# Optimization experiments

Hardware: AMD Instinct MI355X
Metric: run time of the kernel (lower is better)

Reference implementation:

```python
import jax, jax.numpy as jnp
import numpy as np

NC = 19
CH16, CH32 = 1024, 2048
B, H, W = 4, 64, 64
EPS = 1e-5


def bn_relu(x, gamma, beta):
    # Train-mode BatchNorm (batch statistics, as in torch default) + ReLU.
    axes = (0,) + tuple(range(2, x.ndim))  # reduce over batch + spatial
    mean = jnp.mean(x, axes, keepdims=True)
    var = jnp.var(x, axes, keepdims=True)
    shp = (1, -1) + (1,) * (x.ndim - 2)
    return jax.nn.relu((x - mean) * jax.lax.rsqrt(var + EPS) * gamma.reshape(shp) + beta.reshape(shp))


def setup_inputs() -> dict:
    key = jax.random.key(0)
    ks = jax.random.split(key, 10)
    def p(k, shape, fan):
        return jax.random.normal(k, shape, jnp.float32) / np.float32(np.sqrt(fan))
    ones = lambda c: jnp.ones((c,), jnp.float32)
    zeros = lambda c: jnp.zeros((c,), jnp.float32)
    return {
        "x": jax.random.normal(ks[0], (B, CH32, H, W), jnp.float32),
        "low_level_feature": jax.random.normal(ks[1], (B, CH16, H, W), jnp.float32),
        "W_L": p(ks[2], (NC, CH16), CH16), "b_L": zeros(NC),
        "W_X": p(ks[3], (512, CH32, 3, 3), CH32 * 9), "g_X": ones(512), "be_X": zeros(512),
        "W_phi": p(ks[4], (256, 512), 512), "g_phi": ones(256), "be_phi": zeros(256),
        "W_psi": p(ks[5], (256, 512), 512), "g_psi": ones(256), "be_psi": zeros(256),
        "W_delta": p(ks[6], (256, 512), 512), "g_delta": ones(256), "be_delta": zeros(256),
        "W_rho": p(ks[7], (512, 256), 256), "g_rho": ones(512), "be_rho": zeros(512),
        "W_g": p(ks[8], (512, 1024), 1024), "g_g": ones(512), "be_g": zeros(512),
        "W_out": p(ks[9], (NC, 512), 512), "b_out": zeros(NC),
    }


def reference(x, low_level_feature, W_L, b_L, W_X, g_X, be_X,
              W_phi, g_phi, be_phi, W_psi, g_psi, be_psi,
              W_delta, g_delta, be_delta, W_rho, g_rho, be_rho,
              W_g, g_g, be_g, W_out, b_out):
    b, _, h, w = x.shape
    # X = conv2d(2048->512, 3x3) + BN + ReLU
    Xf = jax.lax.conv_general_dilated(x, W_X, (1, 1), 'SAME',
                                      dimension_numbers=('NCHW', 'OIHW', 'NCHW'))
    Xf = bn_relu(Xf, g_X, be_X)                          # [b,512,h,w]
    # L = 1x1 conv (with bias) -> soft object regions
    L = jnp.einsum('bchw,nc->bnhw', low_level_feature, W_L) + b_L[None, :, None, None]
    l_flat = L.reshape(b, L.shape[1], -1)                # [b,nc,N]
    M = jax.nn.softmax(l_flat, axis=-1)                  # softmax over N
    X_flat = Xf.reshape(b, 512, -1)                      # [b,512,N]
    # f_k = (M @ X_flat^T)^T : object region features [b,512,nc]
    f_k = jnp.einsum('bkn,bcn->bck', M, X_flat)
    # phi/psi/delta: 1x1 conv1d + BN + ReLU
    query = bn_relu(jnp.einsum('oc,bck->bok', W_phi, f_k), g_phi, be_phi)      # [b,256,nc]
    key_ = bn_relu(jnp.einsum('oc,bcn->bon', W_psi, X_flat), g_psi, be_psi)    # [b,256,N]
    logit = jnp.einsum('bqk,bqn->bkn', query, key_)      # [b,nc,N]
    attn = jax.nn.softmax(logit, axis=1)                 # softmax over nc (dim 1)
    delta = bn_relu(jnp.einsum('oc,bck->bok', W_delta, f_k), g_delta, be_delta)  # [b,256,nc]
    attn_sum = jnp.einsum('bqk,bkn->bqn', delta, attn)   # [b,256,N]
    X_obj = bn_relu(jnp.einsum('oq,bqn->bon', W_rho, attn_sum), g_rho, be_rho)
    X_obj = X_obj.reshape(b, 512, h, w)
    concat = jnp.concatenate([Xf, X_obj], axis=1)        # [b,1024,h,w]
    X_bar = bn_relu(jnp.einsum('oc,bchw->bohw', W_g, concat), g_g, be_g)
    out = jnp.einsum('nc,bchw->bnhw', W_out, X_bar) + b_out[None, :, None, None]
    return out
```

## Files before the change

kernel.cpp:

```cpp
#include <hip/hip_runtime.h>
#include <hip/hip_bf16.h>
#include <cstdint>
#include <cstddef>

#define EPSV 1e-5f

typedef float f32x4 __attribute__((ext_vector_type(4)));
typedef _Float16 f16x8 __attribute__((ext_vector_type(8)));
typedef unsigned short ushortx8 __attribute__((ext_vector_type(8)));

__device__ __forceinline__ unsigned short f2h(float f) {
  _Float16 h = (_Float16)f;
  return *reinterpret_cast<unsigned short*>(&h);
}

__device__ __forceinline__ void gload16(const void* g, void* l) {
  __builtin_amdgcn_global_load_lds(
      (const __attribute__((address_space(1))) void*)g,
      (__attribute__((address_space(3))) void*)l, 16, 0, 0);
}

__global__ __launch_bounds__(256) void ocr_halo_zero(unsigned short* __restrict__ xT) {
  int e = blockIdx.x, b = blockIdx.y, t = threadIdx.x;
  ushortx8 z = {0, 0, 0, 0, 0, 0, 0, 0};
  if (e < 2) {
    int row = e ? 65 : 0;
    ushortx8* p = (ushortx8*)(xT + (size_t)(b * 66 + row) * 66 * 2048);
    for (int i = t; i < 66 * 256; i += 256) p[i] = z;
  } else {
    int col = (e == 3) ? 65 : 0;
    for (int idx = t; idx < 64 * 256; idx += 256) {
      int r = (idx >> 8) + 1, v = idx & 255;
      ((ushortx8*)(xT + ((size_t)(b * 66 + r) * 66 + col) * 2048))[v] = z;
    }
  }
}

__global__ __launch_bounds__(256) void ocr_cvt_x(const float* __restrict__ x,
                                                 unsigned short* __restrict__ xT) {
  __shared__ float tile[64][65];
  int icb = blockIdx.x, h = blockIdx.y, b = blockIdx.z, t = threadIdx.x;
  const float* xp = x + ((size_t)b * 2048 + icb * 64) * 4096 + h * 64;
  #pragma unroll
  for (int r = 0; r < 16; ++r) {
    int icl = r * 4 + (t >> 6), w = t & 63;
    tile[icl][w] = xp[(size_t)icl * 4096 + w];
  }
  __syncthreads();
  #pragma unroll
  for (int it = 0; it < 2; ++it) {
    int w = it * 32 + (t >> 3), cb = (t & 7) * 8;
    ushortx8 o;
    #pragma unroll
    for (int j = 0; j < 8; ++j) o[j] = f2h(tile[cb + j][w]);
    *(ushortx8*)&xT[(((size_t)b * 66 + h + 1) * 66 + (w + 1)) * 2048 + icb * 64 + cb] = o;
  }
}

__global__ __launch_bounds__(256) void ocr_cvt_w(const float* __restrict__ Wx,
                                                 unsigned short* __restrict__ WT) {
  int oc = blockIdx.x >> 3;
  int ic = (blockIdx.x & 7) * 256 + threadIdx.x;
  const float* wp = Wx + ((size_t)oc * 2048 + ic) * 9;
  float v[9];
  #pragma unroll
  for (int t = 0; t < 9; ++t) v[t] = wp[t];
  #pragma unroll
  for (int t = 0; t < 9; ++t)
    WT[((size_t)t * 512 + oc) * 2048 + ic] = f2h(v[t]);
}

__global__ __launch_bounds__(256) void ocr_cvt_h2(const float* __restrict__ inA,
                                                  unsigned short* __restrict__ outA,
                                                  const float* __restrict__ inB,
                                                  unsigned short* __restrict__ outB) {
  int i = blockIdx.x * 256 + threadIdx.x;
  if (i < 131072) outA[i] = f2h(inA[i]);
  if (i < 524288) outB[i] = f2h(inB[i]);
}

__global__ __launch_bounds__(512, 4) void ocr_conv_mfma(const unsigned short* __restrict__ xT,
                                                        const unsigned short* __restrict__ WT,
                                                        float* __restrict__ Xf) {
  __shared__ __align__(16) char lds_raw[65536];
  float* red = (float*)lds_raw;

  const int t = threadIdx.x;
  const int wv = t >> 6, lane = t & 63;
  const int kg = lane >> 4, lc = lane & 15;
  const int ws = wv & 3, kh = wv >> 2;

  const int bx = blockIdx.x;
  const int hg  = ((bx & 7) << 1) | ((bx >> 3) & 1);
  const int b   = (bx >> 4) & 3;
  const int oct = bx >> 6;
  const int oc0 = oct * 64, h0 = hg * 4;

  const char* gp[8]; int lo[8]; bool go[8];
  #pragma unroll
  for (int i = 0; i < 8; ++i) {
    int c = wv * 8 + i;
    go[i] = c < 63;
    int cc = go[i] ? c : 0;
    if (cc < 38) {
      int cell = cc * 64 + lane; if (cell > 2375) cell = 2375;
      int r = cell / 66, col = cell - r * 66; if (col > 63) col = 63;
      int tap = r >> 2, kgs = r & 3;
      gp[i] = (const char*)WT + (size_t)(((tap * 512 + oc0 + col) * 2048) + kgs * 8) * 2;
      lo[i] = cc * 1024;
    } else {
      int c2 = cc - 38;
      int cell = c2 * 64 + lane; if (cell > 1583) cell = 1583;
      int r = cell / 66, col = cell - r * 66;
      int row = r >> 2, kgs = r & 3;
      gp[i] = (const char*)xT + (size_t)((((b * 66 + h0 + row) * 66 + col) * 2048) + kgs * 8) * 2;
      lo[i] = 38912 + c2 * 1024;
    }
  }

  f32x4 acc[4][4] = {};

  #pragma unroll
  for (int i = 0; i < 8; ++i) if (go[i]) gload16(gp[i], lds_raw + lo[i]);
  __syncthreads();

  #pragma unroll 1
  for (int step = 0; step < 64; ++step) {
    const short* As = (const short*)lds_raw;
    const short* Bs = (const short*)(lds_raw + 38912);
    #pragma unroll
    for (int j = 0; j < 5; ++j) {
      const int tap = kh * 4 + j;
      const int dh = tap / 3, dw = tap - dh * 3;
      f16x8 av[4];
      #pragma unroll
      for (int mi = 0; mi < 4; ++mi)
        av[mi] = *(const f16x8*)&As[((tap * 4 + kg) * 66 + mi * 16 + lc) * 8];
      const int row = ws + dh;
      const int nw0 = (tap == 4) ? (kh ? 2 : 0) : 0;
      const int nwN = (tap == 4) ? (nw0 + 2) : 4;
      #pragma unroll
      for (int nw = 0; nw < 4; ++nw) {
        if (nw >= nw0 && nw < nwN) {
          f16x8 bv = *(const f16x8*)&Bs[((row * 4 + kg) * 66 + nw * 16 + lc + dw) * 8];
          #pragma unroll
          for (int mi = 0; mi < 4; ++mi)
            acc[mi][nw] = __builtin_amdgcn_mfma_f32_16x16x32_f16(av[mi], bv, acc[mi][nw], 0, 0, 0);
        }
      }
    }
    if (step < 63) {
      __syncthreads();
      unsigned adv = (unsigned)(step + 1) * 64u;
      #pragma unroll
      for (int i = 0; i < 8; ++i) if (go[i]) gload16(gp[i] + adv, lds_raw + lo[i]);
      __syncthreads();
    }
  }

  __syncthreads();
  if (kh == 1) {
    #pragma unroll
    for (int mi = 0; mi < 4; ++mi)
      #pragma unroll
      for (int nw = 0; nw < 4; ++nw)
        *(f32x4*)&red[(((ws * 16 + mi * 4 + nw) * 64) + lane) * 4] = acc[mi][nw];
  }
  __syncthreads();
  if (kh == 0) {
    const int h = h0 + ws;
    #pragma unroll
    for (int mi = 0; mi < 4; ++mi) {
      #pragma unroll
      for (int nw = 0; nw < 4; ++nw) {
        f32x4 other = *(const f32x4*)&red[(((ws * 16 + mi * 4 + nw) * 64) + lane) * 4];
        f32x4 s = acc[mi][nw] + other;
        #pragma unroll
        for (int r = 0; r < 4; ++r) {
          int oc = oc0 + mi * 16 + (lane >> 4) * 4 + r;
          int w = nw * 16 + lc;
          Xf[(((size_t)b * 512 + oc) * 64 + h) * 64 + w] = s[r];
        }
      }
    }
  }
}

template<int K, int OT, int NT, int NWM, int NWN, int LDB>
__global__ __launch_bounds__(256) void ocr_gemm_h(const unsigned short* __restrict__ Ah,
                                                  const unsigned short* __restrict__ Bh,
                                                  float* __restrict__ Cm, int O) {
  static_assert(NT == 128, "NT fixed");
  constexpr int MI = OT / NWM / 16;
  constexpr int NI = NT / NWN / 16;
  constexpr int SA = OT + 2, SB = NT + 2;
  constexpr int ACELL = 4 * OT / 256;
  constexpr int ABUF = 4 * SA * 8;
  constexpr int BBUF = 4 * SB * 8;
  constexpr int NS = K / 32;
  constexpr int LPW = ACELL + 2;
  __shared__ __align__(16) short As_s[2 * ABUF];
  __shared__ __align__(16) short Bs_s[2 * BBUF];

  const int t = threadIdx.x;
  const int wv = t >> 6, lane = t & 63;
  const int kg = lane >> 4, lc = lane & 15;
  const int wm = wv / NWN, wn = wv % NWN;

  const int n0 = blockIdx.x * NT, o0 = blockIdx.y * OT, b = blockIdx.z;

  const char* aBase[ACELL]; int aLds[ACELL];
  #pragma unroll
  for (int r = 0; r < ACELL; ++r) {
    int flat0 = r * 256 + (t & 448);
    int flat  = flat0 + lane;
    int kgs = flat / OT, ol = flat % OT;
    aBase[r] = (const char*)(Ah + ((size_t)(o0 + ol)) * K + kgs * 8);
    aLds[r] = ((flat0 / OT) * SA + (flat0 % OT)) * 16;
  }
  const char* bBase[2]; int bLds[2];
  #pragma unroll
  for (int r = 0; r < 2; ++r) {
    int flat0 = r * 256 + (t & 448);
    int flat  = flat0 + lane;
    int kgs = flat >> 7, nl = flat & 127;
    bBase[r] = (const char*)(Bh + ((size_t)b * 4096 + n0 + nl) * LDB + kgs * 8);
    bLds[r] = ((flat0 >> 7) * SB + (flat0 & 127)) * 16;
  }

  f32x4 acc[MI][NI] = {};
  #pragma unroll
  for (int r = 0; r < ACELL; ++r) gload16(aBase[r], (char*)As_s + aLds[r]);
  #pragma unroll
  for (int r = 0; r < 2; ++r) gload16(bBase[r], (char*)Bs_s + bLds[r]);
  asm volatile("s_waitcnt vmcnt(0)" ::: "memory");
  __builtin_amdgcn_s_barrier();

  int cur = 0;
  #pragma unroll 1
  for (int step = 0; step < NS; ++step) {
    if (step + 1 < NS) {
      unsigned adv = (unsigned)(step + 1) * 64u;
      int nA = (cur ^ 1) * ABUF * 2, nB = (cur ^ 1) * BBUF * 2;
      #pragma unroll
      for (int r = 0; r < ACELL; ++r) gload16(aBase[r] + adv, (char*)As_s + nA + aLds[r]);
      #pragma unroll
      for (int r = 0; r < 2; ++r) gload16(bBase[r] + adv, (char*)Bs_s + nB + bLds[r]);
      if constexpr (LPW == 3) asm volatile("s_waitcnt vmcnt(3)" ::: "memory");
      else                    asm volatile("s_waitcnt vmcnt(4)" ::: "memory");
    } else {
      asm volatile("s_waitcnt vmcnt(0)" ::: "memory");
    }
    __builtin_amdgcn_s_barrier();

    const short* As = As_s + cur * ABUF;
    const short* Bsc = Bs_s + cur * BBUF;
    f16x8 av[MI], bv[NI];
    #pragma unroll
    for (int mi = 0; mi < MI; ++mi)
      av[mi] = *(const f16x8*)&As[(kg * SA + wm * (MI * 16) + mi * 16 + lc) * 8];
    #pragma unroll
    for (int ni = 0; ni < NI; ++ni)
      bv[ni] = *(const f16x8*)&Bsc[(kg * SB + wn * (NI * 16) + ni * 16 + lc) * 8];
    __builtin_amdgcn_s_setprio(1);
    #pragma unroll
    for (int mi = 0; mi < MI; ++mi)
      #pragma unroll
      for (int ni = 0; ni < NI; ++ni)
        acc[mi][ni] = __builtin_amdgcn_mfma_f32_16x16x32_f16(av[mi], bv[ni], acc[mi][ni], 0, 0, 0);
    __builtin_amdgcn_s_setprio(0);
    asm volatile("s_waitcnt lgkmcnt(0)" ::: "memory");
    __builtin_amdgcn_sched_barrier(0);
    __builtin_amdgcn_s_barrier();
    cur ^= 1;
  }
  #pragma unroll
  for (int mi = 0; mi < MI; ++mi) {
    #pragma unroll
    for (int ni = 0; ni < NI; ++ni) {
      int n = n0 + wn * (NI * 16) + ni * 16 + lc;
      #pragma unroll
      for (int r = 0; r < 4; ++r) {
        int oc = o0 + wm * (MI * 16) + mi * 16 + (lane >> 4) * 4 + r;
        Cm[((size_t)b * O + oc) * 4096 + n] = acc[mi][ni][r];
      }
    }
  }
}

__global__ __launch_bounds__(256) void ocr_t2h(const float* __restrict__ in,
                                               const float* __restrict__ scale,
                                               const float* __restrict__ shift,
                                               unsigned short* __restrict__ out,
                                               int C, int coff) {
  __shared__ float tile[64][65];
  int n0 = blockIdx.x * 64, c0 = blockIdx.y * 64, b = blockIdx.z;
  int t = threadIdx.x;
  #pragma unroll
  for (int r = 0; r < 16; ++r) {
    int c_l = r * 4 + (t >> 6), n_l = t & 63;
    tile[c_l][n_l] = in[((size_t)(b * C + c0 + c_l)) * 4096 + n0 + n_l];
  }
  __syncthreads();
  int n_l = t >> 2, cb = (t & 3) * 16;
  ushortx8 o0v, o1v;
  #pragma unroll
  for (int j = 0; j < 8; ++j) {
    int c = c0 + cb + j;
    o0v[j] = f2h(fmaxf(0.f, tile[cb + j][n_l] * scale[c] + shift[c]));
  }
  #pragma unroll
  for (int j = 0; j < 8; ++j) {
    int c = c0 + cb + 8 + j;
    o1v[j] = f2h(fmaxf(0.f, tile[cb + 8 + j][n_l] * scale[c] + shift[c]));
  }
  size_t base = ((size_t)b * 4096 + n0 + n_l) * 1024 + coff + c0 + cb;
  *(ushortx8*)&out[base] = o0v;
  *(ushortx8*)&out[base + 8] = o1v;
}

__global__ __launch_bounds__(256) void ocr_chan_stats(const float* __restrict__ buf,
                                                      const float* __restrict__ gamma,
                                                      const float* __restrict__ beta,
                                                      float* __restrict__ scale,
                                                      float* __restrict__ shift, int C) {
  int c = blockIdx.x, t = threadIdx.x;
  float s = 0.f, q = 0.f;
  for (int b = 0; b < 4; ++b) {
    const float* p = buf + ((size_t)b * C + c) * 4096;
    for (int i = t; i < 4096; i += 256) { float v = p[i]; s += v; q += v * v; }
  }
  __shared__ float ls[256], lq[256];
  ls[t] = s; lq[t] = q; __syncthreads();
  for (int off = 128; off > 0; off >>= 1) {
    if (t < off) { ls[t] += ls[t + off]; lq[t] += lq[t + off]; }
    __syncthreads();
  }
  if (t == 0) {
    float mean = ls[0] / 16384.f;
    float var  = lq[0] / 16384.f - mean * mean;
    float sc   = gamma[c] * rsqrtf(var + EPSV);
    scale[c] = sc; shift[c] = beta[c] - mean * sc;
  }
}

__global__ __launch_bounds__(256) void ocr_lproj(const float* __restrict__ llf,
                                                 const float* __restrict__ WL,
                                                 const float* __restrict__ bL,
                                                 float* __restrict__ L) {
  int h = blockIdx.x, b = blockIdx.y;
  int t = threadIdx.x, w = t & 63, csub = t >> 6;
  float acc[19];
  #pragma unroll
  for (int k = 0; k < 19; ++k) acc[k] = 0.f;
  const float* base = llf + ((size_t)b * 1024 + csub * 256) * 4096 + h * 64 + w;
  #pragma unroll 1
  for (int c4 = 0; c4 < 64; ++c4) {
    float lv[4];
    #pragma unroll
    for (int i = 0; i < 4; ++i) lv[i] = base[(size_t)(c4 + i * 64) * 4096];
    #pragma unroll
    for (int i = 0; i < 4; ++i) {
      const float* wl = &WL[csub * 256 + c4 + i * 64];
      #pragma unroll
      for (int k = 0; k < 19; ++k) acc[k] += wl[k * 1024] * lv[i];
    }
  }
  __shared__ float red[4][64][19];
  #pragma unroll
  for (int k = 0; k < 19; ++k) red[csub][w][k] = acc[k];
  __syncthreads();
  if (csub == 0) {
    #pragma unroll
    for (int k = 0; k < 19; ++k) {
      float s = red[0][w][k] + red[1][w][k] + red[2][w][k] + red[3][w][k] + bL[k];
      L[((size_t)b * 19 + k) * 4096 + h * 64 + w] = s;
    }
  }
}

__global__ __launch_bounds__(256) void ocr_softmax4096(float* __restrict__ buf) {
  int row = blockIdx.x, t = threadIdx.x;
  float* p = buf + (size_t)row * 4096;
  __shared__ float ls[256];
  float m = -1e30f;
  for (int i = t; i < 4096; i += 256) m = fmaxf(m, p[i]);
  ls[t] = m; __syncthreads();
  for (int off = 128; off > 0; off >>= 1) { if (t < off) ls[t] = fmaxf(ls[t], ls[t + off]); __syncthreads(); }
  m = ls[0]; __syncthreads();
  float s = 0.f;
  for (int i = t; i < 4096; i += 256) { float e = __expf(p[i] - m); p[i] = e; s += e; }
  ls[t] = s; __syncthreads();
  for (int off = 128; off > 0; off >>= 1) { if (t < off) ls[t] += ls[t + off]; __syncthreads(); }
  float inv = 1.f / ls[0];
  for (int i = t; i < 4096; i += 256) p[i] *= inv;
}

__global__ __launch_bounds__(256) void ocr_fk(const float* __restrict__ M,
                                              const float* __restrict__ Xf,
                                              const float* __restrict__ scale,
                                              const float* __restrict__ shift,
                                              float* __restrict__ fk) {
  int c = blockIdx.x, b = blockIdx.y, t = threadIdx.x;
  float acc[19];
  #pragma unroll
  for (int k = 0; k < 19; ++k) acc[k] = 0.f;
  const float* xp = Xf + ((size_t)b * 512 + c) * 4096;
  const float* mp = M + (size_t)b * 19 * 4096;
  float sc = scale[c], sh = shift[c];
  for (int n = t; n < 4096; n += 256) {
    float xv = fmaxf(0.f, xp[n] * sc + sh);
    #pragma unroll
    for (int k = 0; k < 19; ++k) acc[k] += mp[k * 4096 + n] * xv;
  }
  __shared__ float red[19 * 256];
  #pragma unroll
  for (int k = 0; k < 19; ++k) red[k * 256 + t] = acc[k];
  __syncthreads();
  for (int off = 128; off > 0; off >>= 1) {
    if (t < off) {
      #pragma unroll
      for (int k = 0; k < 19; ++k) red[k * 256 + t] += red[k * 256 + t + off];
    }
    __syncthreads();
  }
  if (t < 19) fk[((size_t)b * 512 + c) * 19 + t] = red[t * 256];
}

__global__ __launch_bounds__(256) void ocr_qd2(const float* __restrict__ Wphi,
                                               const float* __restrict__ Wdelta,
                                               const float* __restrict__ fk,
                                               float* __restrict__ qry,
                                               float* __restrict__ dlt) {
  int blk = blockIdx.x;
  const float* Wm = (blk < 76) ? Wphi : Wdelta;
  float* out = (blk < 76) ? qry : dlt;
  int tid = (blk < 76 ? blk : blk - 76) * 256 + threadIdx.x;
  if (tid >= 4 * 256 * 19) return;
  int k = tid % 19, o = (tid / 19) % 256, b = tid / (19 * 256);
  const float* fp = fk + (size_t)b * 512 * 19 + k;
  const float* wp = Wm + (size_t)o * 512;
  float acc = 0.f;
  for (int c = 0; c < 512; ++c) acc += wp[c] * fp[c * 19];
  out[tid] = acc;
}

__global__ __launch_bounds__(128) void ocr_bn76x2(float* __restrict__ qry,
                                                  float* __restrict__ dlt,
                                                  const float* __restrict__ g_phi,
                                                  const float* __restrict__ be_phi,
                                                  const float* __restrict__ g_delta,
                                                  const float* __restrict__ be_delta) {
  bool second = blockIdx.x >= 256;
  int o = blockIdx.x & 255, t = threadIdx.x;
  float* buf = second ? dlt : qry;
  const float* gamma = second ? g_delta : g_phi;
  const float* beta  = second ? be_delta : be_phi;
  bool act = t < 76;
  float v = 0.f;
  size_t idx = 0;
  if (act) {
    int b = t / 19, k = t % 19;
    idx = ((size_t)b * 256 + o) * 19 + k;
    v = buf[idx];
  }
  __shared__ float ls[128], lq[128];
  ls[t] = act ? v : 0.f; lq[t] = act ? v * v : 0.f; __syncthreads();
  for (int off = 64; off > 0; off >>= 1) { if (t < off) { ls[t] += ls[t + off]; lq[t] += lq[t + off]; } __syncthreads(); }
  __shared__ float s_sc, s_sh;
  if (t == 0) {
    float mean = ls[0] / 76.f;
    float var  = lq[0] / 76.f - mean * mean;
    float sc   = gamma[o] * rsqrtf(var + EPSV);
    s_sc = sc; s_sh = beta[o] - mean * sc;
  }
  __syncthreads();
  if (act) buf[idx] = fmaxf(0.f, v * s_sc + s_sh);
}

__global__ __launch_bounds__(256) void ocr_attn(const float* __restrict__ query,
                                                const float* __restrict__ key,
                                                const float* __restrict__ scale,
                                                const float* __restrict__ shift,
                                                float* __restrict__ attn) {
  int n0 = blockIdx.x * 64, b = blockIdx.y;
  int t = threadIdx.x, nl = t & 63, qsub = t >> 6;
  __shared__ float ql[256 * 19];
  for (int i = t; i < 256 * 19; i += 256) ql[i] = query[(size_t)b * 256 * 19 + i];
  __syncthreads();
  float acc[19];
  #pragma unroll
  for (int k = 0; k < 19; ++k) acc[k] = 0.f;
  const float* kp = key + ((size_t)b * 256 + qsub * 64) * 4096 + n0 + nl;
  #pragma unroll 1
  for (int q4 = 0; q4 < 64; q4 += 4) {
    float kv[4];
    #pragma unroll
    for (int i = 0; i < 4; ++i) kv[i] = kp[(size_t)(q4 + i) * 4096];
    #pragma unroll
    for (int i = 0; i < 4; ++i) {
      int ch = qsub * 64 + q4 + i;
      float kva = fmaxf(0.f, kv[i] * scale[ch] + shift[ch]);
      const float* qq = &ql[ch * 19];
      #pragma unroll
      for (int k = 0; k < 19; ++k) acc[k] += qq[k] * kva;
    }
  }
  __shared__ float red[4][64][19];
  #pragma unroll
  for (int k = 0; k < 19; ++k) red[qsub][nl][k] = acc[k];
  __syncthreads();
  if (qsub == 0) {
    float v[19]; float m = -1e30f;
    #pragma unroll
    for (int k = 0; k < 19; ++k) {
      v[k] = red[0][nl][k] + red[1][nl][k] + red[2][nl][k] + red[3][nl][k];
      m = fmaxf(m, v[k]);
    }
    float s = 0.f;
    #pragma unroll
    for (int k = 0; k < 19; ++k) { v[k] = __expf(v[k] - m); s += v[k]; }
    float inv = 1.f / s;
    #pragma unroll
    for (int k = 0; k < 19; ++k)
      attn[((size_t)b * 19 + k) * 4096 + n0 + nl] = v[k] * inv;
  }
}

__global__ __launch_bounds__(256) void ocr_wd(const float* __restrict__ Wrho,
                                              const float* __restrict__ dlt,
                                              float* __restrict__ Wd) {
  int tid = blockIdx.x * 256 + threadIdx.x;
  if (tid >= 4 * 512 * 19) return;
  int k = tid % 19, o = (tid / 19) % 512, b = tid / (19 * 512);
  const float* dp = dlt + (size_t)b * 256 * 19 + k;
  const float* wp = Wrho + (size_t)o * 256;
  float acc = 0.f;
  for (int q = 0; q < 256; ++q) acc += wp[q] * dp[q * 19];
  Wd[tid] = acc;
}

__global__ __launch_bounds__(384) void ocr_gram(const float* __restrict__ attn,
                                                float* __restrict__ G,
                                                float* __restrict__ RS) {
  __shared__ float al[19][513];
  int n0 = blockIdx.x * 512, b = blockIdx.y, t = threadIdx.x;
  for (int i = t; i < 19 * 512; i += 384) {
    int k = i >> 9, n = i & 511;
    al[k][n] = attn[((size_t)b * 19 + k) * 4096 + n0 + n];
  }
  __syncthreads();
  if (t < 361) {
    int k1 = t / 19, k2 = t % 19;
    float s = 0.f;
    for (int n = 0; n < 512; ++n) s += al[k1][n] * al[k2][n];
    atomicAdd(&G[(b * 19 + k1) * 19 + k2], s);
  } else if (t < 380) {
    int k = t - 361;
    float s = 0.f;
    for (int n = 0; n < 512; ++n) s += al[k][n];
    atomicAdd(&RS[b * 19 + k], s);
  }
}

__global__ __launch_bounds__(512) void ocr_xobj_fin(const float* __restrict__ Wd,
                                                    const float* __restrict__ G,
                                                    const float* __restrict__ RS,
                                                    const float* __restrict__ gamma,
                                                    const float* __restrict__ beta,
                                                    float* __restrict__ scale,
                                                    float* __restrict__ shift) {
  int o = threadIdx.x;
  float s = 0.f, q = 0.f;
  for (int b = 0; b < 4; ++b) {
    float wd[19];
    #pragma unroll
    for (int k = 0; k < 19; ++k) wd[k] = Wd[((size_t)b * 512 + o) * 19 + k];
    const float* g = &G[b * 361];
    const float* rs = &RS[b * 19];
    #pragma unroll
    for (int k = 0; k < 19; ++k) s += wd[k] * rs[k];
    for (int k1 = 0; k1 < 19; ++k1) {
      float tacc = 0.f;
      #pragma unroll
      for (int k2 = 0; k2 < 19; ++k2) tacc += g[k1 * 19 + k2] * wd[k2];
      q += wd[k1] * tacc;
    }
  }
  float mean = s / 16384.f;
  float var  = q / 16384.f - mean * mean;
  float sc   = gamma[o] * rsqrtf(var + EPSV);
  scale[o] = sc; shift[o] = beta[o] - mean * sc;
}

__global__ __launch_bounds__(512) void ocr_xobj_apply(const float* __restrict__ Wd,
                                                      const float* __restrict__ attn,
                                                      const float* __restrict__ scale,
                                                      const float* __restrict__ shift,
                                                      unsigned short* __restrict__ ch) {
  __shared__ float al[19][256];
  int n0 = blockIdx.x * 256, b = blockIdx.y, o = threadIdx.x;
  for (int idx = o; idx < 19 * 256; idx += 512) {
    int k = idx >> 8, nl = idx & 255;
    al[k][nl] = attn[((size_t)b * 19 + k) * 4096 + n0 + nl];
  }
  float wd[19];
  #pragma unroll
  for (int k = 0; k < 19; ++k) wd[k] = Wd[((size_t)b * 512 + o) * 19 + k];
  float sc = scale[o], sh = shift[o];
  __syncthreads();
  #pragma unroll 1
  for (int nl = 0; nl < 256; ++nl) {
    float v = 0.f;
    #pragma unroll
    for (int k = 0; k < 19; ++k) v += wd[k] * al[k][nl];
    v = fmaxf(0.f, v * sc + sh);
    ch[((size_t)b * 4096 + n0 + nl) * 1024 + 512 + o] = f2h(v);
  }
}

__global__ __launch_bounds__(256) void ocr_out(const float* __restrict__ Wout,
                                               const float* __restrict__ bout,
                                               const float* __restrict__ Xbar,
                                               const float* __restrict__ scale,
                                               const float* __restrict__ shift,
                                               float* __restrict__ out) {
  int n0 = blockIdx.x * 64, b = blockIdx.y;
  int t = threadIdx.x, nl = t & 63, csub = t >> 6;
  float acc[19];
  #pragma unroll
  for (int k = 0; k < 19; ++k) acc[k] = 0.f;
  const float* base = Xbar + ((size_t)b * 512 + csub * 128) * 4096 + n0 + nl;
  #pragma unroll 1
  for (int c4 = 0; c4 < 128; c4 += 4) {
    float xv[4];
    #pragma unroll
    for (int i = 0; i < 4; ++i) xv[i] = base[(size_t)(c4 + i) * 4096];
    #pragma unroll
    for (int i = 0; i < 4; ++i) {
      int chn = csub * 128 + c4 + i;
      float a = fmaxf(0.f, xv[i] * scale[chn] + shift[chn]);
      #pragma unroll
      for (int k = 0; k < 19; ++k) acc[k] += Wout[k * 512 + chn] * a;
    }
  }
  __shared__ float red[4][64][19];
  #pragma unroll
  for (int k = 0; k < 19; ++k) red[csub][nl][k] = acc[k];
  __syncthreads();
  if (csub == 0) {
    #pragma unroll
    for (int k = 0; k < 19; ++k) {
      float s = red[0][nl][k] + red[1][nl][k] + red[2][nl][k] + red[3][nl][k] + bout[k];
      out[((size_t)b * 19 + k) * 4096 + n0 + nl] = s;
    }
  }
}

extern "C" void kernel_launch(void* const* d_in, const int* in_sizes, int n_in,
                              void* d_out, int out_size, void* d_ws, size_t ws_size,
                              hipStream_t stream) {
  const float* x    = (const float*)d_in[0];
  const float* llf  = (const float*)d_in[1];
  const float* W_L  = (const float*)d_in[2];
  const float* b_L  = (const float*)d_in[3];
  const float* W_X  = (const float*)d_in[4];
  const float* g_X  = (const float*)d_in[5];
  const float* be_X = (const float*)d_in[6];
  const float* W_phi = (const float*)d_in[7];
  const float* g_phi = (const float*)d_in[8];
  const float* be_phi = (const float*)d_in[9];
  const float* W_psi = (const float*)d_in[10];
  const float* g_psi = (const float*)d_in[11];
  const float* be_psi = (const float*)d_in[12];
  const float* W_delta = (const float*)d_in[13];
  const float* g_delta = (const float*)d_in[14];
  const float* be_delta = (const float*)d_in[15];
  const float* W_rho = (const float*)d_in[16];
  const float* g_rho = (const float*)d_in[17];
  const float* be_rho = (const float*)d_in[18];
  const float* W_g  = (const float*)d_in[19];
  const float* g_g  = (const float*)d_in[20];
  const float* be_g = (const float*)d_in[21];
  const float* W_out = (const float*)d_in[22];
  const float* b_out = (const float*)d_in[23];

  float* ws = (float*)d_ws;
  float* Xf = ws;
  float* U  = ws + 8388608;
  unsigned short* xT = (unsigned short*)U;
  unsigned short* WT = (unsigned short*)(U + 17842176);
  unsigned short* concat_h = (unsigned short*)U;
  float* key  = U + 8388608;
  float* Xbar = U + 12582912;
  float* SM   = U + 22560768;
  float* M     = SM;
  float* attnb = SM + 311296;
  float* fk    = SM + 622592;
  float* qry   = SM + 661504;
  float* dlt   = SM + 680960;
  float* Wd    = SM + 700416;
  float* st    = SM + 739328;
  unsigned short* Wpsi_h = (unsigned short*)(SM + 743424);
  unsigned short* Wg_h   = (unsigned short*)(SM + 808960);
  float* Gm    = SM + 1071104;
  float* RSm   = SM + 1072548;
  float* scX = st,        *shX = st + 512;
  float* scP = st + 1024, *shP = st + 1280;
  float* scR = st + 1536, *shR = st + 2048;
  float* scG = st + 2560, *shG = st + 3072;

  ocr_halo_zero<<<dim3(4, 4), 256, 0, stream>>>(xT);
  ocr_cvt_x<<<dim3(32, 64, 4), 256, 0, stream>>>(x, xT);
  ocr_cvt_w<<<dim3(4096), 256, 0, stream>>>(W_X, WT);
  ocr_cvt_h2<<<dim3(2048), 256, 0, stream>>>(W_psi, Wpsi_h, W_g, Wg_h);
  hipMemsetAsync(Gm, 0, 1520 * sizeof(float), stream);

  ocr_conv_mfma<<<dim3(512), 512, 0, stream>>>(xT, WT, Xf);

  ocr_chan_stats<<<dim3(512), 256, 0, stream>>>(Xf, g_X, be_X, scX, shX, 512);
  ocr_t2h<<<dim3(64, 8, 4), 256, 0, stream>>>(Xf, scX, shX, concat_h, 512, 0);
  ocr_lproj<<<dim3(64, 4), 256, 0, stream>>>(llf, W_L, b_L, M);
  ocr_softmax4096<<<dim3(76), 256, 0, stream>>>(M);
  ocr_fk<<<dim3(512, 4), 256, 0, stream>>>(M, Xf, scX, shX, fk);
  ocr_qd2<<<dim3(152), 256, 0, stream>>>(W_phi, W_delta, fk, qry, dlt);
  ocr_bn76x2<<<dim3(512), 128, 0, stream>>>(qry, dlt, g_phi, be_phi, g_delta, be_delta);
  ocr_gemm_h<512, 64, 128, 2, 2, 1024><<<dim3(32, 4, 4), 256, 0, stream>>>(Wpsi_h, concat_h, key, 256);
  ocr_chan_stats<<<dim3(256), 256, 0, stream>>>(key, g_psi, be_psi, scP, shP, 256);
  ocr_attn<<<dim3(64, 4), 256, 0, stream>>>(qry, key, scP, shP, attnb);
  ocr_wd<<<dim3(152), 256, 0, stream>>>(W_rho, dlt, Wd);
  ocr_gram<<<dim3(8, 4), 384, 0, stream>>>(attnb, Gm, RSm);
  ocr_xobj_fin<<<dim3(1), 512, 0, stream>>>(Wd, Gm, RSm, g_rho, be_rho, scR, shR);
  ocr_xobj_apply<<<dim3(16, 4), 512, 0, stream>>>(Wd, attnb, scR, shR, concat_h);
  ocr_gemm_h<1024, 128, 128, 2, 2, 1024><<<dim3(32, 4, 4), 256, 0, stream>>>(Wg_h, concat_h, Xbar, 512);
  ocr_chan_stats<<<dim3(512), 256, 0, stream>>>(Xbar, g_g, be_g, scG, shG, 512);
  ocr_out<<<dim3(64, 4), 256, 0, stream>>>(W_out, b_out, Xbar, scG, shG, (float*)d_out);
}
```

Measured before the change: 815.3 us.

## Double-buffer conv LDS tiles and enlarge spatial tile to eight rows

The 3x3 conv MFMA kernel now uses 12 waves per block, each handling 3 taps (one kernel row) over two output rows, with a block tile of 8 output rows by 64 output channels. LDS holds two buffers (about 158 KB), so the next K-step's global-to-LDS loads are issued before computing on the current buffer, which removes one of the two barriers per step. The larger spatial tile reuses each weight tile across more rows, and the three tap-groups' partials are reduced through LDS in two stages. The risks are one block per CU because of the LDS size, higher register pressure from 32 accumulators per wave, and only 256 blocks to fill the GPU.

Measured after the change: 874.1 us. +7.2%, slower.

```diff
diff --git a/kernel.cpp b/kernel.cpp
--- a/kernel.cpp
+++ b/kernel.cpp
@@ -79,102 +79,112 @@
   if (i < 524288) outB[i] = f2h(inB[i]);
 }
 
-__global__ __launch_bounds__(512, 4) void ocr_conv_mfma(const unsigned short* __restrict__ xT,
+__global__ __launch_bounds__(768, 3) void ocr_conv_mfma(const unsigned short* __restrict__ xT,
                                                         const unsigned short* __restrict__ WT,
                                                         float* __restrict__ Xf) {
-  __shared__ __align__(16) char lds_raw[65536];
+  __shared__ __align__(16) char lds_raw[161792];
   float* red = (float*)lds_raw;
 
   const int t = threadIdx.x;
   const int wv = t >> 6, lane = t & 63;
   const int kg = lane >> 4, lc = lane & 15;
-  const int ws = wv & 3, kh = wv >> 2;
+  const int ws = wv & 3, tt = wv >> 2;
 
   const int bx = blockIdx.x;
-  const int hg  = ((bx & 7) << 1) | ((bx >> 3) & 1);
-  const int b   = (bx >> 4) & 3;
-  const int oct = bx >> 6;
-  const int oc0 = oct * 64, h0 = hg * 4;
-
-  const char* gp[8]; int lo[8]; bool go[8];
-  #pragma unroll
-  for (int i = 0; i < 8; ++i) {
-    int c = wv * 8 + i;
-    go[i] = c < 63;
+  const int hg  = bx & 7;
+  const int b   = (bx >> 3) & 3;
+  const int oct = bx >> 5;
+  const int oc0 = oct * 64, h0 = hg * 8;
+
+  const char* gp[7]; int lo[7]; bool go[7];
+  #pragma unroll
+  for (int i = 0; i < 7; ++i) {
+    int c = wv * 7 + i;
+    go[i] = c < 79;
     int cc = go[i] ? c : 0;
-    if (cc < 38) {
-      int cell = cc * 64 + lane; if (cell > 2375) cell = 2375;
-      int r = cell / 66, col = cell - r * 66; if (col > 63) col = 63;
+    if (cc < 37) {
+      int cell = cc * 64 + lane; if (cell > 2339) cell = 2339;
+      int r = cell / 65, col = cell - r * 65; if (col > 63) col = 63;
       int tap = r >> 2, kgs = r & 3;
       gp[i] = (const char*)WT + (size_t)(((tap * 512 + oc0 + col) * 2048) + kgs * 8) * 2;
       lo[i] = cc * 1024;
     } else {
-      int c2 = cc - 38;
-      int cell = c2 * 64 + lane; if (cell > 1583) cell = 1583;
+      int c2 = cc - 37;
+      int cell = c2 * 64 + lane; if (cell > 2639) cell = 2639;
       int r = cell / 66, col = cell - r * 66;
       int row = r >> 2, kgs = r & 3;
       gp[i] = (const char*)xT + (size_t)((((b * 66 + h0 + row) * 66 + col) * 2048) + kgs * 8) * 2;
-      lo[i] = 38912 + c2 * 1024;
-    }
-  }
-
-  f32x4 acc[4][4] = {};
-
-  #pragma unroll
-  for (int i = 0; i < 8; ++i) if (go[i]) gload16(gp[i], lds_raw + lo[i]);
-  __syncthreads();
-
+      lo[i] = 37888 + c2 * 1024;
+    }
+  }
+
+  f32x4 acc[4][8] = {};
+
+  #pragma unroll
+  for (int i = 0; i < 7; ++i) if (go[i]) gload16(gp[i], lds_raw + lo[i]);
+  __syncthreads();
+
+  int cur = 0;
   #pragma unroll 1
   for (int step = 0; step < 64; ++step) {
-    const short* As = (const short*)lds_raw;
-    const short* Bs = (const short*)(lds_raw + 38912);
-    #pragma unroll
-    for (int j = 0; j < 5; ++j) {
-      const int tap = kh * 4 + j;
-      const int dh = tap / 3, dw = tap - dh * 3;
+    if (step < 63) {
+      unsigned adv = (unsigned)(step + 1) * 64u;
+      int nxt = (cur ^ 1) * 80896;
+      #pragma unroll
+      for (int i = 0; i < 7; ++i) if (go[i]) gload16(gp[i] + adv, lds_raw + nxt + lo[i]);
+    }
+    const short* As = (const short*)(lds_raw + cur * 80896);
+    const short* Bs = (const short*)(lds_raw + cur * 80896 + 37888);
+    #pragma unroll
+    for (int j = 0; j < 3; ++j) {
+      const int tap = tt * 3 + j;
       f16x8 av[4];
       #pragma unroll
       for (int mi = 0; mi < 4; ++mi)
-        av[mi] = *(const f16x8*)&As[((tap * 4 + kg) * 66 + mi * 16 + lc) * 8];
-      const int row = ws + dh;
-      const int nw0 = (tap == 4) ? (kh ? 2 : 0) : 0;
-      const int nwN = (tap == 4) ? (nw0 + 2) : 4;
-      #pragma unroll
-      for (int nw = 0; nw < 4; ++nw) {
-        if (nw >= nw0 && nw < nwN) {
-          f16x8 bv = *(const f16x8*)&Bs[((row * 4 + kg) * 66 + nw * 16 + lc + dw) * 8];
+        av[mi] = *(const f16x8*)&As[((tap * 4 + kg) * 65 + mi * 16 + lc) * 8];
+      #pragma unroll
+      for (int hh = 0; hh < 2; ++hh) {
+        const int row = 2 * ws + hh + tt;
+        #pragma unroll
+        for (int nw = 0; nw < 4; ++nw) {
+          f16x8 bv = *(const f16x8*)&Bs[((row * 4 + kg) * 66 + nw * 16 + lc + j) * 8];
           #pragma unroll
           for (int mi = 0; mi < 4; ++mi)
-            acc[mi][nw] = __builtin_amdgcn_mfma_f32_16x16x32_f16(av[mi], bv, acc[mi][nw], 0, 0, 0);
+            acc[mi][hh * 4 + nw] = __builtin_amdgcn_mfma_f32_16x16x32_f16(av[mi], bv, acc[mi][hh * 4 + nw], 0, 0, 0);
         }
       }
     }
-    if (step < 63) {
-      __syncthreads();
-      unsigned adv = (unsigned)(step + 1) * 64u;
-      #pragma unroll
-      for (int i = 0; i < 8; ++i) if (go[i]) gload16(gp[i] + adv, lds_raw + lo[i]);
-      __syncthreads();
-    }
-  }
-
-  __syncthreads();
-  if (kh == 1) {
+    __syncthreads();
+    cur ^= 1;
+  }
+
+  if (tt == 2) {
     #pragma unroll
     for (int mi = 0; mi < 4; ++mi)
       #pragma unroll
-      for (int nw = 0; nw < 4; ++nw)
-        *(f32x4*)&red[(((ws * 16 + mi * 4 + nw) * 64) + lane) * 4] = acc[mi][nw];
-  }
-  __syncthreads();
-  if (kh == 0) {
-    const int h = h0 + ws;
+      for (int ni = 0; ni < 8; ++ni)
+        *(f32x4*)&red[((ws * 32 + mi * 8 + ni) * 64 + lane) * 4] = acc[mi][ni];
+  }
+  __syncthreads();
+  if (tt == 1) {
+    #pragma unroll
+    for (int mi = 0; mi < 4; ++mi)
+      #pragma unroll
+      for (int ni = 0; ni < 8; ++ni) {
+        f32x4 o = *(const f32x4*)&red[((ws * 32 + mi * 8 + ni) * 64 + lane) * 4];
+        *(f32x4*)&red[((ws * 32 + mi * 8 + ni) * 64 + lane) * 4] = acc[mi][ni] + o;
+      }
+  }
+  __syncthreads();
+  if (tt == 0) {
     #pragma unroll
     for (int mi = 0; mi < 4; ++mi) {
       #pragma unroll
-      for (int nw = 0; nw < 4; ++nw) {
-        f32x4 other = *(const f32x4*)&red[(((ws * 16 + mi * 4 + nw) * 64) + lane) * 4];
-        f32x4 s = acc[mi][nw] + other;
+      for (int ni = 0; ni < 8; ++ni) {
+        f32x4 o = *(const f32x4*)&red[((ws * 32 + mi * 8 + ni) * 64 + lane) * 4];
+        f32x4 s = acc[mi][ni] + o;
+        int hh = ni >> 2, nw = ni & 3;
+        int h = h0 + 2 * ws + hh;
         #pragma unroll
         for (int r = 0; r < 4; ++r) {
           int oc = oc0 + mi * 16 + (lane >> 4) * 4 + r;
@@ -716,7 +726,7 @@
   ocr_cvt_h2<<<dim3(2048), 256, 0, stream>>>(W_psi, Wpsi_h, W_g, Wg_h);
   hipMemsetAsync(Gm, 0, 1520 * sizeof(float), stream);
 
-  ocr_conv_mfma<<<dim3(512), 512, 0, stream>>>(xT, WT, Xf);
+  ocr_conv_mfma<<<dim3(256), 768, 0, stream>>>(xT, WT, Xf);
 
   ocr_chan_stats<<<dim3(512), 256, 0, stream>>>(Xf, g_X, be_X, scX, shX, 512);
   ocr_t2h<<<dim3(64, 8, 4), 256, 0, stream>>>(Xf, scX, shX, concat_h, 512, 0);
```

## Double-buffer conv LDS tiles and enlarge block to eight output rows

Applied to the files above, without the earlier changes.

The 3x3 conv MFMA kernel now runs 1024-thread blocks that each cover eight output rows instead of four, using 160KB of LDS split into two buffers. The loads for the next K-step are issued before computing on the current buffer, so each step needs one barrier instead of two and global-to-LDS traffic overlaps the MFMAs. Each weight tile is also reused across more rows, which cuts the halo and weight load overhead. The cost is one block per CU with the full LDS, which lowers occupancy and leaves latency hiding to the prefetch alone.

After: 737.4 us (median of 2 runs). -9.6%, faster.

```diff
diff --git a/kernel.cpp b/kernel.cpp
--- a/kernel.cpp
+++ b/kernel.cpp
@@ -79,55 +79,58 @@
   if (i < 524288) outB[i] = f2h(inB[i]);
 }
 
-__global__ __launch_bounds__(512, 4) void ocr_conv_mfma(const unsigned short* __restrict__ xT,
-                                                        const unsigned short* __restrict__ WT,
-                                                        float* __restrict__ Xf) {
-  __shared__ __align__(16) char lds_raw[65536];
+__global__ __launch_bounds__(1024, 4) void ocr_conv_mfma(const unsigned short* __restrict__ xT,
+                                                         const unsigned short* __restrict__ WT,
+                                                         float* __restrict__ Xf) {
+  __shared__ __align__(16) char lds_raw[163840];
   float* red = (float*)lds_raw;
 
   const int t = threadIdx.x;
   const int wv = t >> 6, lane = t & 63;
   const int kg = lane >> 4, lc = lane & 15;
-  const int ws = wv & 3, kh = wv >> 2;
-
-  const int bx = blockIdx.x;
-  const int hg  = ((bx & 7) << 1) | ((bx >> 3) & 1);
-  const int b   = (bx >> 4) & 3;
-  const int oct = bx >> 6;
-  const int oc0 = oct * 64, h0 = hg * 4;
-
-  const char* gp[8]; int lo[8]; bool go[8];
-  #pragma unroll
-  for (int i = 0; i < 8; ++i) {
-    int c = wv * 8 + i;
-    go[i] = c < 63;
-    int cc = go[i] ? c : 0;
-    if (cc < 38) {
-      int cell = cc * 64 + lane; if (cell > 2375) cell = 2375;
+  const int ws = wv & 7, kh = wv >> 3;
+
+  const int hg  = blockIdx.x & 7;
+  const int b   = (blockIdx.x >> 3) & 3;
+  const int oct = blockIdx.x >> 5;
+  const int oc0 = oct * 64, h0 = hg * 8;
+
+  const char* gp[5]; int lo[5];
+  #pragma unroll
+  for (int i = 0; i < 5; ++i) {
+    int c = wv * 5 + i;
+    lo[i] = c * 1024;
+    if (c < 38) {
+      int cell = c * 64 + lane; if (cell > 2375) cell = 2375;
       int r = cell / 66, col = cell - r * 66; if (col > 63) col = 63;
       int tap = r >> 2, kgs = r & 3;
       gp[i] = (const char*)WT + (size_t)(((tap * 512 + oc0 + col) * 2048) + kgs * 8) * 2;
-      lo[i] = cc * 1024;
     } else {
-      int c2 = cc - 38;
-      int cell = c2 * 64 + lane; if (cell > 1583) cell = 1583;
+      int c2 = c - 38;
+      int cell = c2 * 64 + lane; if (cell > 2639) cell = 2639;
       int r = cell / 66, col = cell - r * 66;
       int row = r >> 2, kgs = r & 3;
       gp[i] = (const char*)xT + (size_t)((((b * 66 + h0 + row) * 66 + col) * 2048) + kgs * 8) * 2;
-      lo[i] = 38912 + c2 * 1024;
     }
   }
 
   f32x4 acc[4][4] = {};
 
   #pragma unroll
-  for (int i = 0; i < 8; ++i) if (go[i]) gload16(gp[i], lds_raw + lo[i]);
-  __syncthreads();
-
+  for (int i = 0; i < 5; ++i) gload16(gp[i], lds_raw + lo[i]);
+  __syncthreads();
+
+  int cur = 0;
   #pragma unroll 1
   for (int step = 0; step < 64; ++step) {
-    const short* As = (const short*)lds_raw;
-    const short* Bs = (const short*)(lds_raw + 38912);
+    if (step < 63) {
+      unsigned adv = (unsigned)(step + 1) * 64u;
+      int nxt = (cur ^ 1) * 81920;
+      #pragma unroll
+      for (int i = 0; i < 5; ++i) gload16(gp[i] + adv, lds_raw + nxt + lo[i]);
+    }
+    const short* As = (const short*)(lds_raw + cur * 81920);
+    const short* Bs = (const short*)(lds_raw + cur * 81920 + 38912);
     #pragma unroll
     for (int j = 0; j < 5; ++j) {
       const int tap = kh * 4 + j;
@@ -149,16 +152,10 @@
         }
       }
     }
-    if (step < 63) {
-      __syncthreads();
-      unsigned adv = (unsigned)(step + 1) * 64u;
-      #pragma unroll
-      for (int i = 0; i < 8; ++i) if (go[i]) gload16(gp[i] + adv, lds_raw + lo[i]);
-      __syncthreads();
-    }
-  }
-
-  __syncthreads();
+    __syncthreads();
+    cur ^= 1;
+  }
+
   if (kh == 1) {
     #pragma unroll
     for (int mi = 0; mi < 4; ++mi)
@@ -716,7 +713,7 @@
   ocr_cvt_h2<<<dim3(2048), 256, 0, stream>>>(W_psi, Wpsi_h, W_g, Wg_h);
   hipMemsetAsync(Gm, 0, 1520 * sizeof(float), stream);
 
-  ocr_conv_mfma<<<dim3(512), 512, 0, stream>>>(xT, WT, Xf);
+  ocr_conv_mfma<<<dim3(256), 1024, 0, stream>>>(xT, WT, Xf);
 
   ocr_chan_stats<<<dim3(512), 256, 0, stream>>>(Xf, g_X, be_X, scX, shX, 512);
   ocr_t2h<<<dim3(64, 8, 4), 256, 0, stream>>>(Xf, scX, shX, concat_h, 512, 0);
```
